# Optimization experiments

Hardware: AMD Instinct MI355X
Metric: run time of the kernel (lower is better)

The kernel has to match this reference:

```python
import jax, jax.numpy as jnp
import numpy as np

DT = 0.001
TAU_M = 0.02
TAU_S = 0.005
ALPHA = 1.0 - DT / TAU_S  # synaptic decay = 0.8
BETA = 1.0 - DT / TAU_M   # membrane decay = 0.95


def setup_inputs() -> dict:
    key = jax.random.key(0)
    k1, k2 = jax.random.split(key)
    steps, batch, d1, d2 = 100, 256, 784, 512
    x = (jax.random.uniform(k1, (steps, batch, d1)) < 0.05).astype(jnp.float32)
    # kaiming_normal_ on (d2, d1): std = sqrt(2 / fan_in)
    weight = jax.random.normal(k2, (d2, d1), dtype=jnp.float32) * np.float32(np.sqrt(2.0 / d1))
    return {"x": x, "weight": weight}


def reference(x, weight):
    # x: [steps, batch, d1] spikes; weight: [d2, d1]
    batch = x.shape[1]
    d2 = weight.shape[0]
    zeros = jnp.zeros((batch, d2), dtype=x.dtype)

    def step(carry, x_t):
        I_prev, V_prev = carry
        I = ALPHA * I_prev + x_t @ weight.T            # synaptic current
        V_pre = BETA * V_prev + (1.0 - BETA) * I        # membrane before reset
        s = (V_pre > 1.0).astype(x.dtype)               # threshold crossing
        V = (1.0 - s) * V_pre                           # reset to zero on spike
        return (I, V), s

    # torch loop runs i = 1..steps-1 using input[i-1]; output[0] stays zero
    _, spikes = jax.lax.scan(step, (zeros, zeros), x[:-1])
    return jnp.concatenate([zeros[None], spikes], axis=0)  # [steps, batch, d2]
```

## Files before the change

kernel.cpp:

```cpp
#include <hip/hip_runtime.h>

#define STEPS 100
#define BATCH 256
#define D1 784
#define D1P 785
#define D2 512
#define NSTEP 99
#define NTB (NSTEP * BATCH)
#define LIST_PAD 80

#define JS 32
#define ZBW (D1P * JS)
#define FUSED_LDS ((ZBW + 2 * 8 * 16 * JS) * 4)
#define NWIN 13

#define L1_LISTS_OFF 0
#define L1_LISTS_BYTES ((size_t)NTB * LIST_PAD * 2)
#define L1_CNTS_OFF  L1_LISTS_BYTES
#define L1_CNTS_BYTES ((size_t)NTB * 4)
#define WS_T1        (L1_CNTS_OFF + L1_CNTS_BYTES)

#define WT_BYTES  (D1P * D2 * 4)
#define T2_Z_OFF  ((size_t)((WT_BYTES + 255) & ~255))
#define Z_BYTES   ((size_t)NTB * D2 * 4)
#define WS_T2     (T2_Z_OFF + Z_BYTES)

#define HALF1 392
#define HCAP  64


__global__ __launch_bounds__(256) void prep_lists(
    const float* __restrict__ x, unsigned short* __restrict__ lists,
    unsigned int* __restrict__ cnt16s)
{
    const int wid  = blockIdx.x * 4 + (threadIdx.x >> 6);
    const int lane = threadIdx.x & 63;
    const float* xt = x + (size_t)wid * D1;
    unsigned short* lp = lists + (size_t)wid * LIST_PAD;
    const unsigned long long lt = (1ull << lane) - 1ull;

    int cnt = 0;
    for (int base = 0; base < D1; base += 256) {
        const int i0 = base + lane * 4;
        float4 v = make_float4(0.f, 0.f, 0.f, 0.f);
        if (i0 < D1) v = *(const float4*)(xt + i0);
        const bool a0 = v.x > 0.5f, a1 = v.y > 0.5f;
        const bool a2 = v.z > 0.5f, a3 = v.w > 0.5f;
        const unsigned long long m0 = __ballot(a0);
        const unsigned long long m1 = __ballot(a1);
        const unsigned long long m2 = __ballot(a2);
        const unsigned long long m3 = __ballot(a3);
        int p = cnt + __popcll(m0 & lt) + __popcll(m1 & lt)
                    + __popcll(m2 & lt) + __popcll(m3 & lt);
        if (a0) { if (p < LIST_PAD) lp[p] = (unsigned short)((i0 + 0) << 3); ++p; }
        if (a1) { if (p < LIST_PAD) lp[p] = (unsigned short)((i0 + 1) << 3); ++p; }
        if (a2) { if (p < LIST_PAD) lp[p] = (unsigned short)((i0 + 2) << 3); ++p; }
        if (a3) { if (p < LIST_PAD) lp[p] = (unsigned short)((i0 + 3) << 3); ++p; }
        cnt += __popcll(m0) + __popcll(m1) + __popcll(m2) + __popcll(m3);
    }
    if (cnt > LIST_PAD) cnt = LIST_PAD;
    int cnt16 = (cnt + 15) & ~15;
    if (cnt16 < 16) cnt16 = 16;
    if (lane < cnt16 - cnt) lp[cnt + lane] = (unsigned short)(D1 << 3);
    if (lane == 0) cnt16s[wid] = (unsigned int)cnt16;
}

#define RD16(t) (*(const float4*)(base + ((((unsigned)(t)) << 4) + \
                 (qd16 ^ ((((unsigned)(t)) << 1) & 0x70u)))))

#define READS8(d0,d1,d2,d3,d4,d5,d6,d7,e)                                      \
    d0 = RD16(e.x & 0xFFFFu);  d1 = RD16(e.x >> 16);                           \
    d2 = RD16(e.y & 0xFFFFu);  d3 = RD16(e.y >> 16);                           \
    d4 = RD16(e.z & 0xFFFFu);  d5 = RD16(e.z >> 16);                           \
    d6 = RD16(e.w & 0xFFFFu);  d7 = RD16(e.w >> 16);

#define ACC8(p0,p1,p2,p3,p4,p5,p6,p7)                                          \
    ax += p0.x; ay += p0.y; az += p0.z; aw += p0.w;                            \
    bx += p1.x; by += p1.y; bz += p1.z; bw += p1.w;                            \
    ax += p2.x; ay += p2.y; az += p2.z; aw += p2.w;                            \
    bx += p3.x; by += p3.y; bz += p3.z; bw += p3.w;                            \
    ax += p4.x; ay += p4.y; az += p4.z; aw += p4.w;                            \
    bx += p5.x; by += p5.y; bz += p5.z; bw += p5.w;                            \
    ax += p6.x; ay += p6.y; az += p6.z; aw += p6.w;                            \
    bx += p7.x; by += p7.y; bz += p7.z; bw += p7.w;

__global__ __launch_bounds__(1024, 4) void gather_lif(
    const float* __restrict__ W,
    const unsigned short* __restrict__ lists,
    const unsigned int* __restrict__ cnt16s,
    float* __restrict__ out)
{
    const int slice  = blockIdx.x & 15;
    const int bchunk = blockIdx.x >> 4;
    const int j0 = slice * JS;
    const int b0 = bchunk * 16;

    extern __shared__ float wt[];

    {
        const int jj = threadIdx.x & 31;
        const int q4 = jj & 28;
        const int c  = jj & 3;
        const int ih = threadIdx.x >> 5;
        const float* wrow = W + (size_t)(j0 + jj) * D1;
        for (int i4 = ih; i4 < 196; i4 += 32) {
            int i = i4 * 4;
            float4 v = *(const float4*)(wrow + i);
            wt[(i + 0) * JS + ((q4 ^ (((i + 0) & 7) << 2)) | c)] = v.x;
            wt[(i + 1) * JS + ((q4 ^ (((i + 1) & 7) << 2)) | c)] = v.y;
            wt[(i + 2) * JS + ((q4 ^ (((i + 2) & 7) << 2)) | c)] = v.z;
            wt[(i + 3) * JS + ((q4 ^ (((i + 3) & 7) << 2)) | c)] = v.w;
        }
        if (threadIdx.x < JS) wt[D1 * JS + threadIdx.x] = 0.f;
    }

    const int lane = threadIdx.x & 63;
    const int wv   = threadIdx.x >> 6;
    const int toff = wv >> 1;
    const int grp  = lane >> 3;
    const int bi   = ((wv & 1) << 3) | grp;
    const int myb  = b0 + bi;
    const unsigned qd16 = (unsigned)((lane & 7) << 4);
    const char* base = (const char*)wt;

    float I = 0.f, V = 0.f;
    size_t obase = 0;
    if (threadIdx.x < 512) {
        obase = (size_t)(b0 + (threadIdx.x >> 5)) * D2 + j0 + (threadIdx.x & 31);
        out[obase] = 0.f;
    }

    int tb0 = toff * BATCH + myb;
    uint4 cE0 = *(const uint4*)(lists + (size_t)tb0 * LIST_PAD);
    uint4 cE1 = *(const uint4*)(lists + (size_t)tb0 * LIST_PAD + 8);
    int   cC  = (int)cnt16s[tb0];

    __syncthreads();

    for (int w = 0; w < NWIN; ++w) {
        int tn = (w + 1) * 8 + toff;
        if (tn > NSTEP - 1) tn = NSTEP - 1;
        const size_t tbn = (size_t)tn * BATCH + myb;
        uint4 nE0 = *(const uint4*)(lists + tbn * LIST_PAD);
        uint4 nE1 = *(const uint4*)(lists + tbn * LIST_PAD + 8);
        int   nC  = (int)cnt16s[tbn];

        const int t = w * 8 + toff;
        if (t < NSTEP) {
            const unsigned short* lp =
                lists + (size_t)((size_t)t * BATCH + myb) * LIST_PAD;
            const int c16 = cC;
            float4 A0, A1, A2, A3, A4, A5, A6, A7;
            float4 B0, B1, B2, B3, B4, B5, B6, B7;
            READS8(A0, A1, A2, A3, A4, A5, A6, A7, cE0);
            READS8(B0, B1, B2, B3, B4, B5, B6, B7, cE1);
            float ax = 0.f, ay = 0.f, az = 0.f, aw = 0.f;
            float bx = 0.f, by = 0.f, bz = 0.f, bw = 0.f;
            for (int k = 16; k < c16; k += 16) {
                uint4 eA = *(const uint4*)(lp + k);
                uint4 eB = *(const uint4*)(lp + k + 8);
                ACC8(A0, A1, A2, A3, A4, A5, A6, A7)
                READS8(A0, A1, A2, A3, A4, A5, A6, A7, eA);
                ACC8(B0, B1, B2, B3, B4, B5, B6, B7)
                READS8(B0, B1, B2, B3, B4, B5, B6, B7, eB);
            }
            ACC8(A0, A1, A2, A3, A4, A5, A6, A7)
            ACC8(B0, B1, B2, B3, B4, B5, B6, B7)
            float4 r4;
            r4.x = ax + bx; r4.y = ay + by; r4.z = az + bz; r4.w = aw + bw;
            *(float4*)(wt + ZBW + (((w & 1) * 8 + toff) * 512)
                       + bi * JS + ((lane & 7) << 2)) = r4;
        }
        __syncthreads();
        if (threadIdx.x < 512) {
            const int nt = (w == NWIN - 1) ? 3 : 8;
            const float* zb = wt + ZBW + (w & 1) * 4096 + threadIdx.x;
            float* op = out + (size_t)(w * 8 + 1) * (BATCH * D2) + obase;
            for (int u = 0; u < nt; ++u) {
                float zv = zb[(size_t)u * 512];
                I = 0.8f * I + zv;
                float Vp = 0.95f * V + 0.05f * I;
                float s = (Vp > 1.0f) ? 1.0f : 0.f;
                V = (1.0f - s) * Vp;
                op[(size_t)u * (BATCH * D2)] = s;
            }
        }
        cE0 = nE0; cE1 = nE1; cC = nC;
    }
}

__global__ __launch_bounds__(256) void lif_scan(
    const float* __restrict__ z, float* __restrict__ out)
{
    const int gid = blockIdx.x * 256 + threadIdx.x;
    out[gid] = 0.f;
    float I = 0.f, V = 0.f;
    const size_t S = (size_t)BATCH * D2;
    const float* zp = z + gid;
    float* op = out + S + gid;
    float zz[16];
    #pragma unroll
    for (int u = 0; u < 16; ++u) zz[u] = zp[(size_t)u * S];
    for (int t0 = 0; t0 < NSTEP; t0 += 16) {
        float zn[16];
        const int tn = t0 + 16;
        #pragma unroll
        for (int u = 0; u < 16; ++u) {
            zn[u] = 0.f;
            if (tn + u < NSTEP) zn[u] = zp[(size_t)(tn + u) * S];
        }
        const int n = (NSTEP - t0 < 16) ? (NSTEP - t0) : 16;
        #pragma unroll
        for (int u = 0; u < 16; ++u)
            if (u < n) {
                I = 0.8f * I + zz[u];
                float Vp = 0.95f * V + 0.05f * I;
                float s = (Vp > 1.0f) ? 1.0f : 0.f;
                V = (1.0f - s) * Vp;
                op[(size_t)(t0 + u) * S] = s;
            }
        #pragma unroll
        for (int u = 0; u < 16; ++u) zz[u] = zn[u];
    }
}

__global__ void transpose_w(const float* __restrict__ W, float* __restrict__ Wt) {
    __shared__ float tile[32][33];
    int i0 = blockIdx.x * 32;
    int j0 = blockIdx.y * 32;
    int tx = threadIdx.x, ty = threadIdx.y;
    for (int r = 0; r < 32; r += 8) {
        int jj = j0 + ty + r, ii = i0 + tx;
        float v = 0.f;
        if (jj < D2 && ii < D1) v = W[jj * D1 + ii];
        tile[ty + r][tx] = v;
    }
    __syncthreads();
    for (int r = 0; r < 32; r += 8) {
        int ii = i0 + ty + r, jj = j0 + tx;
        if (ii < D1P && jj < D2) Wt[ii * D2 + jj] = tile[tx][ty + r];
    }
}

__global__ __launch_bounds__(512) void gather_z(
    const float* __restrict__ x, const float* __restrict__ Wt,
    float* __restrict__ z)
{
    const int g    = threadIdx.x >> 7;
    const int t128 = threadIdx.x & 127;
    const int half = (threadIdx.x >> 6) & 1;
    const int lane = threadIdx.x & 63;
    const int tb   = blockIdx.x * 4 + g;
    __shared__ __align__(16) unsigned int s_off[4][2][HCAP];
    __shared__ int s_cnt[4][2];
    {
        const float* xh = x + (size_t)tb * D1 + half * HALF1;
        unsigned int* lp = s_off[g][half];
        int cnt = 0;
        for (int base = 0; base < HALF1; base += 64) {
            int i = base + lane;
            bool a = (i < HALF1) && (xh[i] > 0.5f);
            unsigned long long m = __ballot(a);
            int pre = __popcll(m & ((1ull << lane) - 1ull));
            if (a) {
                int p = cnt + pre;
                if (p < HCAP) lp[p] = (unsigned int)((half * HALF1 + i) << 11);
            }
            cnt += __popcll(m);
        }
        if (cnt > HCAP) cnt = HCAP;
        int cnt4 = (cnt + 3) & ~3;
        if (lane < cnt4 - cnt) lp[cnt + lane] = (unsigned int)(D1 << 11);
        if (lane == 0) s_cnt[g][half] = cnt4;
    }
    __syncthreads();
    const char* wj = (const char*)Wt + (t128 << 4);
    float ax0 = 0.f, ay0 = 0.f, az0 = 0.f, aw0 = 0.f;
    float ax1 = 0.f, ay1 = 0.f, az1 = 0.f, aw1 = 0.f;
    #pragma unroll
    for (int h = 0; h < 2; ++h) {
        const unsigned int* l = s_off[g][h];
        const int c4 = s_cnt[g][h];
        for (int k = 0; k < c4; k += 4) {
            uint4 o = *(const uint4*)(l + k);
            float4 w0 = *(const float4*)(wj + o.x);
            float4 w1 = *(const float4*)(wj + o.y);
            float4 w2 = *(const float4*)(wj + o.z);
            float4 w3 = *(const float4*)(wj + o.w);
            ax0 += w0.x; ay0 += w0.y; az0 += w0.z; aw0 += w0.w;
            ax1 += w1.x; ay1 += w1.y; az1 += w1.z; aw1 += w1.w;
            ax0 += w2.x; ay0 += w2.y; az0 += w2.z; aw0 += w2.w;
            ax1 += w3.x; ay1 += w3.y; az1 += w3.z; aw1 += w3.w;
        }
    }
    float4 r;
    r.x = ax0 + ax1; r.y = ay0 + ay1; r.z = az0 + az1; r.w = aw0 + aw1;
    *(float4*)(z + (size_t)tb * D2 + (t128 << 2)) = r;
}

__global__ __launch_bounds__(256) void snn_fallback(
    const float* __restrict__ x, const float* __restrict__ Wfull,
    float* __restrict__ out)
{
    const int b = blockIdx.x >> 1;
    const int jhalf = blockIdx.x & 1;
    const int j = jhalf * 256 + threadIdx.x;
    const int lane = threadIdx.x & 63;
    __shared__ int s_cnt;
    __shared__ int s_list[D1];
    out[(size_t)b * D2 + j] = 0.f;
    float I = 0.f, V = 0.f;
    const float* wrow = Wfull + (size_t)j * D1;
    for (int t = 0; t < STEPS - 1; ++t) {
        if (threadIdx.x == 0) s_cnt = 0;
        __syncthreads();
        const float* xt = x + (size_t)(t * BATCH + b) * D1;
        for (int base = 0; base < D1; base += 256) {
            int i = base + threadIdx.x;
            bool active = (i < D1) && (xt[i] > 0.5f);
            unsigned long long mask = __ballot(active);
            int nact = __popcll(mask);
            int pre = __popcll(mask & ((1ull << lane) - 1ull));
            int wb = 0;
            if (lane == 0 && nact) wb = atomicAdd(&s_cnt, nact);
            wb = __shfl(wb, 0);
            if (active) s_list[wb + pre] = i;
        }
        __syncthreads();
        const int cnt = s_cnt;
        float a0 = 0.f, a1 = 0.f, a2 = 0.f, a3 = 0.f;
        int k = 0;
        for (; k + 4 <= cnt; k += 4) {
            a0 += wrow[s_list[k]];     a1 += wrow[s_list[k + 1]];
            a2 += wrow[s_list[k + 2]]; a3 += wrow[s_list[k + 3]];
        }
        for (; k < cnt; ++k) a0 += wrow[s_list[k]];
        float acc = (a0 + a1) + (a2 + a3);
        I = 0.8f * I + acc;
        float Vp = 0.95f * V + 0.05f * I;
        float s = (Vp > 1.0f) ? 1.0f : 0.f;
        V = (1.0f - s) * Vp;
        out[(size_t)(t + 1) * (BATCH * D2) + (size_t)b * D2 + j] = s;
        __syncthreads();
    }
}

extern "C" void kernel_launch(void* const* d_in, const int* in_sizes, int n_in,
                              void* d_out, int out_size, void* d_ws, size_t ws_size,
                              hipStream_t stream) {
    const float* x = (const float*)d_in[0];
    const float* w = (const float*)d_in[1];
    float* out = (float*)d_out;
    char* ws = (char*)d_ws;

    if (ws_size >= WS_T1) {
        static bool gl_init = false;
        if (!gl_init) {
            (void)hipFuncSetAttribute((const void*)gather_lif,
                hipFuncAttributeMaxDynamicSharedMemorySize, FUSED_LDS);
            gl_init = true;
        }
        unsigned short* lists = (unsigned short*)(ws + L1_LISTS_OFF);
        unsigned int* cnt16s = (unsigned int*)(ws + L1_CNTS_OFF);
        prep_lists<<<NTB / 4, 256, 0, stream>>>(x, lists, cnt16s);
        gather_lif<<<256, 1024, FUSED_LDS, stream>>>(w, lists, cnt16s, out);
    } else if (ws_size >= WS_T2) {
        float* wt = (float*)ws;
        float* z  = (float*)(ws + T2_Z_OFF);
        dim3 tg(25, 16), tb(32, 8);
        transpose_w<<<tg, tb, 0, stream>>>(w, wt);
        gather_z<<<NTB / 4, 512, 0, stream>>>(x, wt, z);
        lif_scan<<<BATCH * D2 / 256, 256, 0, stream>>>(z, out);
    } else {
        snn_fallback<<<BATCH * 2, 256, 0, stream>>>(x, w, out);
    }
}
```

Before: 185.2 us.

## Make each wave own one batch row to drop per-window block barriers

Each of the 16 waves now handles one batch element across 8 timesteps, with one 8-lane group per timestep. It writes its partial sums to a private LDS slice and runs the LIF recurrence inside the wave, so the per-window __syncthreads and the 512-thread scan phase are gone. The LDS XOR swizzle on the weight tile is also removed and the z buffer shrinks. The intent is to remove block-wide synchronisation stalls, at the cost of possible LDS bank conflicts in the gathers. There is also a reliance on wave-synchronous LDS ordering between the z write and the scan read.

```diff
diff --git a/kernel.cpp b/kernel.cpp
--- a/kernel.cpp
+++ b/kernel.cpp
@@ -11,7 +11,7 @@
 
 #define JS 32
 #define ZBW (D1P * JS)
-#define FUSED_LDS ((ZBW + 2 * 8 * 16 * JS) * 4)
+#define FUSED_LDS ((ZBW + 16 * 256) * 4)
 #define NWIN 13
 
 #define L1_LISTS_OFF 0
@@ -65,8 +65,7 @@
     if (lane == 0) cnt16s[wid] = (unsigned int)cnt16;
 }
 
-#define RD16(t) (*(const float4*)(base + ((((unsigned)(t)) << 4) + \
-                 (qd16 ^ ((((unsigned)(t)) << 1) & 0x70u)))))
+#define RD16(t) (*(const float4*)(base + ((((unsigned)(t)) << 4) + qd16)))
 
 #define READS8(d0,d1,d2,d3,d4,d5,d6,d7,e)                                      \
     d0 = RD16(e.x & 0xFFFFu);  d1 = RD16(e.x >> 16);                           \
@@ -99,91 +98,82 @@
 
     {
         const int jj = threadIdx.x & 31;
-        const int q4 = jj & 28;
-        const int c  = jj & 3;
         const int ih = threadIdx.x >> 5;
         const float* wrow = W + (size_t)(j0 + jj) * D1;
         for (int i4 = ih; i4 < 196; i4 += 32) {
             int i = i4 * 4;
             float4 v = *(const float4*)(wrow + i);
-            wt[(i + 0) * JS + ((q4 ^ (((i + 0) & 7) << 2)) | c)] = v.x;
-            wt[(i + 1) * JS + ((q4 ^ (((i + 1) & 7) << 2)) | c)] = v.y;
-            wt[(i + 2) * JS + ((q4 ^ (((i + 2) & 7) << 2)) | c)] = v.z;
-            wt[(i + 3) * JS + ((q4 ^ (((i + 3) & 7) << 2)) | c)] = v.w;
+            wt[(i + 0) * JS + jj] = v.x;
+            wt[(i + 1) * JS + jj] = v.y;
+            wt[(i + 2) * JS + jj] = v.z;
+            wt[(i + 3) * JS + jj] = v.w;
         }
         if (threadIdx.x < JS) wt[D1 * JS + threadIdx.x] = 0.f;
     }
+    __syncthreads();
 
     const int lane = threadIdx.x & 63;
     const int wv   = threadIdx.x >> 6;
-    const int toff = wv >> 1;
     const int grp  = lane >> 3;
-    const int bi   = ((wv & 1) << 3) | grp;
-    const int myb  = b0 + bi;
+    const int myb  = b0 + wv;
     const unsigned qd16 = (unsigned)((lane & 7) << 4);
     const char* base = (const char*)wt;
-
+    float* zw = wt + ZBW + wv * 256;
+
+    const int own = lane & 31;
+    const size_t obase = (size_t)myb * D2 + j0 + own;
+    if (lane < 32) out[obase] = 0.f;
     float I = 0.f, V = 0.f;
-    size_t obase = 0;
-    if (threadIdx.x < 512) {
-        obase = (size_t)(b0 + (threadIdx.x >> 5)) * D2 + j0 + (threadIdx.x & 31);
-        out[obase] = 0.f;
-    }
-
-    int tb0 = toff * BATCH + myb;
-    uint4 cE0 = *(const uint4*)(lists + (size_t)tb0 * LIST_PAD);
-    uint4 cE1 = *(const uint4*)(lists + (size_t)tb0 * LIST_PAD + 8);
+
+    {
+    }
+    const size_t tb0 = (size_t)grp * BATCH + myb;
+    uint4 cE0 = *(const uint4*)(lists + tb0 * LIST_PAD);
+    uint4 cE1 = *(const uint4*)(lists + tb0 * LIST_PAD + 8);
     int   cC  = (int)cnt16s[tb0];
 
-    __syncthreads();
-
     for (int w = 0; w < NWIN; ++w) {
-        int tn = (w + 1) * 8 + toff;
+        int tn = (w + 1) * 8 + grp;
         if (tn > NSTEP - 1) tn = NSTEP - 1;
         const size_t tbn = (size_t)tn * BATCH + myb;
         uint4 nE0 = *(const uint4*)(lists + tbn * LIST_PAD);
         uint4 nE1 = *(const uint4*)(lists + tbn * LIST_PAD + 8);
         int   nC  = (int)cnt16s[tbn];
 
-        const int t = w * 8 + toff;
-        if (t < NSTEP) {
-            const unsigned short* lp =
-                lists + (size_t)((size_t)t * BATCH + myb) * LIST_PAD;
-            const int c16 = cC;
-            float4 A0, A1, A2, A3, A4, A5, A6, A7;
-            float4 B0, B1, B2, B3, B4, B5, B6, B7;
-            READS8(A0, A1, A2, A3, A4, A5, A6, A7, cE0);
-            READS8(B0, B1, B2, B3, B4, B5, B6, B7, cE1);
-            float ax = 0.f, ay = 0.f, az = 0.f, aw = 0.f;
-            float bx = 0.f, by = 0.f, bz = 0.f, bw = 0.f;
-            for (int k = 16; k < c16; k += 16) {
-                uint4 eA = *(const uint4*)(lp + k);
-                uint4 eB = *(const uint4*)(lp + k + 8);
-                ACC8(A0, A1, A2, A3, A4, A5, A6, A7)
-                READS8(A0, A1, A2, A3, A4, A5, A6, A7, eA);
-                ACC8(B0, B1, B2, B3, B4, B5, B6, B7)
-                READS8(B0, B1, B2, B3, B4, B5, B6, B7, eB);
-            }
+        int t = w * 8 + grp;
+        if (t > NSTEP - 1) t = NSTEP - 1;
+        const unsigned short* lp =
+            lists + (size_t)((size_t)t * BATCH + myb) * LIST_PAD;
+        const int c16 = cC;
+        float4 A0, A1, A2, A3, A4, A5, A6, A7;
+        float4 B0, B1, B2, B3, B4, B5, B6, B7;
+        READS8(A0, A1, A2, A3, A4, A5, A6, A7, cE0);
+        READS8(B0, B1, B2, B3, B4, B5, B6, B7, cE1);
+        float ax = 0.f, ay = 0.f, az = 0.f, aw = 0.f;
+        float bx = 0.f, by = 0.f, bz = 0.f, bw = 0.f;
+        for (int k = 16; k < c16; k += 16) {
+            uint4 eA = *(const uint4*)(lp + k);
+            uint4 eB = *(const uint4*)(lp + k + 8);
             ACC8(A0, A1, A2, A3, A4, A5, A6, A7)
+            READS8(A0, A1, A2, A3, A4, A5, A6, A7, eA);
             ACC8(B0, B1, B2, B3, B4, B5, B6, B7)
-            float4 r4;
-            r4.x = ax + bx; r4.y = ay + by; r4.z = az + bz; r4.w = aw + bw;
-            *(float4*)(wt + ZBW + (((w & 1) * 8 + toff) * 512)
-                       + bi * JS + ((lane & 7) << 2)) = r4;
-        }
-        __syncthreads();
-        if (threadIdx.x < 512) {
-            const int nt = (w == NWIN - 1) ? 3 : 8;
-            const float* zb = wt + ZBW + (w & 1) * 4096 + threadIdx.x;
-            float* op = out + (size_t)(w * 8 + 1) * (BATCH * D2) + obase;
-            for (int u = 0; u < nt; ++u) {
-                float zv = zb[(size_t)u * 512];
-                I = 0.8f * I + zv;
-                float Vp = 0.95f * V + 0.05f * I;
-                float s = (Vp > 1.0f) ? 1.0f : 0.f;
-                V = (1.0f - s) * Vp;
-                op[(size_t)u * (BATCH * D2)] = s;
-            }
+            READS8(B0, B1, B2, B3, B4, B5, B6, B7, eB);
+        }
+        ACC8(A0, A1, A2, A3, A4, A5, A6, A7)
+        ACC8(B0, B1, B2, B3, B4, B5, B6, B7)
+        float4 r4;
+        r4.x = ax + bx; r4.y = ay + by; r4.z = az + bz; r4.w = aw + bw;
+        *(float4*)(zw + grp * 32 + ((lane & 7) << 2)) = r4;
+
+        const int nt = (NSTEP - w * 8 < 8) ? (NSTEP - w * 8) : 8;
+        float* op = out + (size_t)(w * 8 + 1) * (BATCH * D2) + obase;
+        for (int u = 0; u < nt; ++u) {
+            float zv = zw[u * 32 + own];
+            I = 0.8f * I + zv;
+            float Vp = 0.95f * V + 0.05f * I;
+            float s = (Vp > 1.0f) ? 1.0f : 0.f;
+            V = (1.0f - s) * Vp;
+            if (lane < 32) op[(size_t)u * (BATCH * D2)] = s;
         }
         cE0 = nE0; cE1 = nE1; cC = nC;
     }
```

Measured after the change: 181.8 us. No clear change (-1.8%).
